# Kernel optimization log

Measured on AMD Instinct MI355X. Metric: run time of the kernel, lower is better.

## Reference

```python
import jax, jax.numpy as jnp
import numpy as np

N_QUBITS = 4
N_LAYERS = 2
ENT = [(i, (i + 1) % N_QUBITS) for i in range(N_QUBITS)]  # fixed entangling ring


def _ry(t):
    c, s = jnp.cos(t / 2), jnp.sin(t / 2)
    return jnp.stack([jnp.stack([c, -s]), jnp.stack([s, c])]).astype(jnp.complex64)


def _rx(t):
    c, s = jnp.cos(t / 2), jnp.sin(t / 2)
    return jnp.stack([jnp.stack([c + 0j, -1j * s]), jnp.stack([-1j * s, c + 0j])]).astype(jnp.complex64)


def _rz(t):
    e = jnp.exp(-0.5j * t.astype(jnp.complex64))
    z = jnp.zeros_like(e)
    return jnp.stack([jnp.stack([e, z]), jnp.stack([z, jnp.conj(e)])])


def _apply_1q(state, U, w):
    # state: (2,)*N_QUBITS; apply 2x2 U on wire w
    s = jnp.moveaxis(state, w, 0)
    s = jnp.tensordot(U, s, ((1,), (0,)))
    return jnp.moveaxis(s, 0, w)


def _cnot(state, c, t):
    s = jnp.moveaxis(state, (c, t), (0, 1))
    s = jnp.concatenate([s[:1], jnp.flip(s[1:], axis=1)], axis=0)
    return jnp.moveaxis(s, (0, 1), (c, t))


def _ansatz(state, vec, params):
    for i in range(N_QUBITS):
        state = _apply_1q(state, _ry(vec[i]), i)
    for l in range(N_LAYERS):
        for i in range(N_QUBITS):
            state = _apply_1q(state, _rx(params[l, i, 0]), i)
            state = _apply_1q(state, _ry(params[l, i, 1]), i)
            state = _apply_1q(state, _rz(params[l, i, 2]), i)
        for a_, b_ in ENT:
            state = _cnot(state, a_, b_)
    return state


def _adjoint_ansatz(state, vec, params):
    # inverse gates in reverse order
    for l in reversed(range(N_LAYERS)):
        for a_, b_ in reversed(ENT):
            state = _cnot(state, a_, b_)  # CNOT is self-inverse
        for i in reversed(range(N_QUBITS)):
            state = _apply_1q(state, _rz(-params[l, i, 2]), i)
            state = _apply_1q(state, _ry(-params[l, i, 1]), i)
            state = _apply_1q(state, _rx(-params[l, i, 0]), i)
    for i in reversed(range(N_QUBITS)):
        state = _apply_1q(state, _ry(-vec[i]), i)
    return state


def setup_inputs() -> dict:
    key = jax.random.key(0)
    k1, k2, k3 = jax.random.split(key, 3)
    a = jax.random.normal(k1, (1024, N_QUBITS), dtype=jnp.float32)
    b = jax.random.normal(k2, (1024, N_QUBITS), dtype=jnp.float32)
    params = jax.random.normal(k3, (N_LAYERS, N_QUBITS, 3), dtype=jnp.float32)
    return {"a": a, "b": b, "params": params}


def reference(a, b, params):
    def pair(x, y):
        psi = jnp.zeros((2,) * N_QUBITS, jnp.complex64).at[(0,) * N_QUBITS].set(1.0)
        psi = _ansatz(psi, x, params)
        psi = _adjoint_ansatz(psi, y, params)
        probs = jnp.abs(psi) ** 2
        # expval of PauliZ on wire 0: +1 for |0>, -1 for |1> on axis 0
        z = jnp.sum(probs[0]) - jnp.sum(probs[1])
        return jnp.abs(z)

    # Gram matrix [len(a), len(b)]
    return jax.vmap(lambda x: jax.vmap(lambda y: pair(x, y))(b))(a)
```

## Files before the change

kernel.cpp:

```cpp
#include <hip/hip_runtime.h>


#define NA 1024
#define NB 1024
#define KD 256
#define RT2 1.41421356237f

typedef __attribute__((ext_vector_type(8))) short bf16x8;
typedef __attribute__((ext_vector_type(4))) float f32x4;

__device__ __forceinline__ unsigned short f2bf(float x) {
    union { float f; unsigned u; } v; v.f = x;
    unsigned r = v.u + 0x7fffu + ((v.u >> 16) & 1u);
    return (unsigned short)(r >> 16);
}

__device__ __forceinline__ uint4 pack8(const float* f) {
    uint4 u;
    u.x = (unsigned)f2bf(f[0]) | ((unsigned)f2bf(f[1]) << 16);
    u.y = (unsigned)f2bf(f[2]) | ((unsigned)f2bf(f[3]) << 16);
    u.z = (unsigned)f2bf(f[4]) | ((unsigned)f2bf(f[5]) << 16);
    u.w = (unsigned)f2bf(f[6]) | ((unsigned)f2bf(f[7]) << 16);
    return u;
}

__device__ __forceinline__ void ry_gate(float* sr, float* si, int w, float t) {
    float s, c; __sincosf(0.5f * t, &s, &c);
    int st = 8 >> w;
    #pragma unroll
    for (int b = 0; b < 16; ++b) {
        if (b & st) continue;
        int j = b | st;
        float r0 = sr[b], i0 = si[b], r1 = sr[j], i1 = si[j];
        sr[b] = c * r0 - s * r1;  si[b] = c * i0 - s * i1;
        sr[j] = s * r0 + c * r1;  si[j] = s * i0 + c * i1;
    }
}

__device__ __forceinline__ void rx_gate(float* sr, float* si, int w, float t) {
    float s, c; __sincosf(0.5f * t, &s, &c);
    int st = 8 >> w;
    #pragma unroll
    for (int b = 0; b < 16; ++b) {
        if (b & st) continue;
        int j = b | st;
        float r0 = sr[b], i0 = si[b], r1 = sr[j], i1 = si[j];
        sr[b] = c * r0 + s * i1;  si[b] = c * i0 - s * r1;
        sr[j] = c * r1 + s * i0;  si[j] = c * i1 - s * r0;
    }
}

__device__ __forceinline__ void rz_gate(float* sr, float* si, int w, float t) {
    float s, c; __sincosf(0.5f * t, &s, &c);
    int st = 8 >> w;
    #pragma unroll
    for (int b = 0; b < 16; ++b) {
        if (b & st) continue;
        int j = b | st;
        float r0 = sr[b], i0 = si[b], r1 = sr[j], i1 = si[j];
        sr[b] = c * r0 + s * i0;  si[b] = c * i0 - s * r0;
        sr[j] = c * r1 - s * i1;  si[j] = c * i1 + s * r1;
    }
}

__device__ __forceinline__ void cnot_gate(float* sr, float* si, int cw, int tw) {
    int cs = 8 >> cw, ts = 8 >> tw;
    #pragma unroll
    for (int b = 0; b < 16; ++b) {
        if ((b & cs) && !(b & ts)) {
            int j = b | ts;
            float tr = sr[b]; sr[b] = sr[j]; sr[j] = tr;
            float ti = si[b]; si[b] = si[j]; si[j] = ti;
        }
    }
}

__device__ __forceinline__ void ansatz(float* sr, float* si, const float* vec, const float* P) {
    #pragma unroll
    for (int q = 0; q < 4; ++q) ry_gate(sr, si, q, vec[q]);
    #pragma unroll
    for (int l = 0; l < 2; ++l) {
        #pragma unroll
        for (int q = 0; q < 4; ++q) {
            rx_gate(sr, si, q, P[l * 12 + q * 3 + 0]);
            ry_gate(sr, si, q, P[l * 12 + q * 3 + 1]);
            rz_gate(sr, si, q, P[l * 12 + q * 3 + 2]);
        }
        cnot_gate(sr, si, 0, 1);
        cnot_gate(sr, si, 1, 2);
        cnot_gate(sr, si, 2, 3);
        cnot_gate(sr, si, 3, 0);
    }
}

__global__ __launch_bounds__(64) void qkm_phase1(
    const float* __restrict__ a, const float* __restrict__ b,
    const float* __restrict__ params,
    uint4* __restrict__ Qv, uint4* __restrict__ Mv) {
    float P[24];
    #pragma unroll
    for (int j = 0; j < 24; ++j) P[j] = params[j];
    int tid = threadIdx.x;
    int blk = blockIdx.x;

    if (blk < 128) {
        __shared__ float Wr[16][64];
        __shared__ float Wi[16][64];
        int g = tid >> 3, t = tid & 7;
        int y = (blk << 3) + g;
        float sr[16], si[16];
        #pragma unroll
        for (int k = 0; k < 16; ++k) { sr[k] = (k == 8 + t) ? 1.f : 0.f; si[k] = 0.f; }
        float vec[4];
        #pragma unroll
        for (int q = 0; q < 4; ++q) vec[q] = b[y * 4 + q];
        ansatz(sr, si, vec, P);
        #pragma unroll
        for (int l = 0; l < 16; ++l) { Wr[l][tid] = sr[l]; Wi[l][tid] = si[l]; }
        __syncthreads();
        int base = g << 3;
        #pragma unroll
        for (int kr = 0; kr < 2; ++kr) {
            int k = 2 * t + kr;
            float re[16], im[16];
            #pragma unroll
            for (int l = 0; l < 16; ++l) { re[l] = 0.f; im[l] = 0.f; }
            #pragma unroll
            for (int p2 = 0; p2 < 8; ++p2) {
                float wrk = Wr[k][base + p2], wik = Wi[k][base + p2];
                #pragma unroll
                for (int l = 0; l < 16; ++l) {
                    float wrl = Wr[l][base + p2], wil = Wi[l][base + p2];
                    re[l] += wrk * wrl + wik * wil;
                    im[l] += wil * wrk - wrl * wik;
                }
            }
            float row[16];
            #pragma unroll
            for (int l = 0; l < 16; ++l) {
                float off = (l < k) ? im[l] : re[l];
                row[l] = (l == k) ? (1.f - 2.f * re[l]) : (-2.f * RT2 * off);
            }
            uint4* d = Mv + y * 32 + k * 2;
            d[0] = pack8(row); d[1] = pack8(row + 8);
        }
    } else if (blk < 144) {
        int i = ((blk - 128) << 6) + tid;
        float sr[16], si[16];
        #pragma unroll
        for (int k = 0; k < 16; ++k) { sr[k] = (k == 0) ? 1.f : 0.f; si[k] = 0.f; }
        float vec[4];
        #pragma unroll
        for (int q = 0; q < 4; ++q) vec[q] = a[i * 4 + q];
        ansatz(sr, si, vec, P);
        #pragma unroll
        for (int k = 0; k < 16; ++k) {
            float rk = sr[k], ik = si[k];
            float row[16];
            #pragma unroll
            for (int l = 0; l < 16; ++l) {
                if (l < k)       row[l] = RT2 * (si[l] * rk - sr[l] * ik);
                else if (l == k) row[l] = rk * rk + ik * ik;
                else             row[l] = RT2 * (rk * sr[l] + ik * si[l]);
            }
            uint4* d = Qv + i * 32 + k * 2;
            d[0] = pack8(row); d[1] = pack8(row + 8);
        }
    }
}

__global__ __launch_bounds__(256) void qkm_phase2(
    const unsigned short* __restrict__ Q, const unsigned short* __restrict__ M,
    float* __restrict__ out) {
    int wave = threadIdx.x >> 6;
    int lane = threadIdx.x & 63;
    int blk = blockIdx.x;
    int xcd = blk & 7;
    int slot = blk >> 3;
    int bi = xcd * 2 + (slot >> 4);
    int bj = slot & 15;
    int wi = wave >> 1, wj = wave & 1;
    int row0 = bi * 64 + wi * 32;
    int col0 = bj * 64 + wj * 32;
    int m16 = lane & 15;
    int quad = lane >> 4;

    const unsigned short* q0 = Q + (size_t)(row0 + m16) * KD + quad * 8;
    const unsigned short* q1 = q0 + 16 * KD;
    const unsigned short* m0 = M + (size_t)(col0 + m16) * KD + quad * 8;
    const unsigned short* m1 = m0 + 16 * KD;

    f32x4 a00 = {0.f,0.f,0.f,0.f}, a01 = {0.f,0.f,0.f,0.f};
    f32x4 a10 = {0.f,0.f,0.f,0.f}, a11 = {0.f,0.f,0.f,0.f};
    #pragma unroll
    for (int kk = 0; kk < 8; ++kk) {
        bf16x8 qa = *(const bf16x8*)(q0 + kk * 32);
        bf16x8 qb = *(const bf16x8*)(q1 + kk * 32);
        bf16x8 ma = *(const bf16x8*)(m0 + kk * 32);
        bf16x8 mb = *(const bf16x8*)(m1 + kk * 32);
        a00 = __builtin_amdgcn_mfma_f32_16x16x32_bf16(qa, ma, a00, 0, 0, 0);
        a01 = __builtin_amdgcn_mfma_f32_16x16x32_bf16(qa, mb, a01, 0, 0, 0);
        a10 = __builtin_amdgcn_mfma_f32_16x16x32_bf16(qb, ma, a10, 0, 0, 0);
        a11 = __builtin_amdgcn_mfma_f32_16x16x32_bf16(qb, mb, a11, 0, 0, 0);
    }
    #pragma unroll
    for (int r = 0; r < 4; ++r) {
        int r0o = row0 + quad * 4 + r;
        int r1o = r0o + 16;
        out[r0o * NB + col0 + m16]      = fabsf(a00[r]);
        out[r0o * NB + col0 + 16 + m16] = fabsf(a01[r]);
        out[r1o * NB + col0 + m16]      = fabsf(a10[r]);
        out[r1o * NB + col0 + 16 + m16] = fabsf(a11[r]);
    }
}

extern "C" void kernel_launch(void* const* d_in, const int* in_sizes, int n_in,
                              void* d_out, int out_size, void* d_ws, size_t ws_size,
                              hipStream_t stream) {
    const float* a = (const float*)d_in[0];
    const float* b = (const float*)d_in[1];
    const float* params = (const float*)d_in[2];
    float* out = (float*)d_out;

    unsigned short* Q = (unsigned short*)d_ws;
    unsigned short* M = Q + (size_t)NA * KD;

    qkm_phase1<<<144, 64, 0, stream>>>(a, b, params, (uint4*)Q, (uint4*)M);
    qkm_phase2<<<256, 256, 0, stream>>>(Q, M, out);
}
```

Baseline: 70.83 us.

## Fuse state prep and MFMA gram into one kernel with LDS-resident Q/M tiles

Merges the two launches into a single kernel. Each 64x64 output tile block recomputes its own 64 a-rows and 64 b-column encodings and stores the bf16 Q/M operands in padded LDS instead of a global workspace. It also precomputes sincos of the parameters once per thread and reuses them across gates. This removes a kernel launch boundary and the global round trip of Q/M, at the cost of 16x redundant ansatz and M construction across blocks and a large dynamic LDS footprint that limits occupancy.

```diff
diff --git a/kernel.cpp b/kernel.cpp
--- a/kernel.cpp
+++ b/kernel.cpp
@@ -3,8 +3,10 @@
 
 #define NA 1024
 #define NB 1024
-#define KD 256
 #define RT2 1.41421356237f
+#define SW 577
+#define SQS 264
+#define LDS_BYTES (16*SW*4*2 + 64*SQS*2*2)
 
 typedef __attribute__((ext_vector_type(8))) short bf16x8;
 typedef __attribute__((ext_vector_type(4))) float f32x4;
@@ -24,8 +26,7 @@
     return u;
 }
 
-__device__ __forceinline__ void ry_gate(float* sr, float* si, int w, float t) {
-    float s, c; __sincosf(0.5f * t, &s, &c);
+__device__ __forceinline__ void ry_cs(float* sr, float* si, int w, float c, float s) {
     int st = 8 >> w;
     #pragma unroll
     for (int b = 0; b < 16; ++b) {
@@ -37,8 +38,7 @@
     }
 }
 
-__device__ __forceinline__ void rx_gate(float* sr, float* si, int w, float t) {
-    float s, c; __sincosf(0.5f * t, &s, &c);
+__device__ __forceinline__ void rx_cs(float* sr, float* si, int w, float c, float s) {
     int st = 8 >> w;
     #pragma unroll
     for (int b = 0; b < 16; ++b) {
@@ -50,8 +50,7 @@
     }
 }
 
-__device__ __forceinline__ void rz_gate(float* sr, float* si, int w, float t) {
-    float s, c; __sincosf(0.5f * t, &s, &c);
+__device__ __forceinline__ void rz_cs(float* sr, float* si, int w, float c, float s) {
     int st = 8 >> w;
     #pragma unroll
     for (int b = 0; b < 16; ++b) {
@@ -75,16 +74,18 @@
     }
 }
 
-__device__ __forceinline__ void ansatz(float* sr, float* si, const float* vec, const float* P) {
-    #pragma unroll
-    for (int q = 0; q < 4; ++q) ry_gate(sr, si, q, vec[q]);
+__device__ __forceinline__ void ansatz_cs(float* sr, float* si,
+                                          const float* vc, const float* vs,
+                                          const float* pc, const float* ps) {
+    #pragma unroll
+    for (int q = 0; q < 4; ++q) ry_cs(sr, si, q, vc[q], vs[q]);
     #pragma unroll
     for (int l = 0; l < 2; ++l) {
         #pragma unroll
         for (int q = 0; q < 4; ++q) {
-            rx_gate(sr, si, q, P[l * 12 + q * 3 + 0]);
-            ry_gate(sr, si, q, P[l * 12 + q * 3 + 1]);
-            rz_gate(sr, si, q, P[l * 12 + q * 3 + 2]);
+            rx_cs(sr, si, q, pc[l*12+q*3+0], ps[l*12+q*3+0]);
+            ry_cs(sr, si, q, pc[l*12+q*3+1], ps[l*12+q*3+1]);
+            rz_cs(sr, si, q, pc[l*12+q*3+2], ps[l*12+q*3+2]);
         }
         cnot_gate(sr, si, 0, 1);
         cnot_gate(sr, si, 1, 2);
@@ -93,66 +94,54 @@
     }
 }
 
-__global__ __launch_bounds__(64) void qkm_phase1(
+__global__ __launch_bounds__(256) void qkm_fused(
     const float* __restrict__ a, const float* __restrict__ b,
-    const float* __restrict__ params,
-    uint4* __restrict__ Qv, uint4* __restrict__ Mv) {
-    float P[24];
-    #pragma unroll
-    for (int j = 0; j < 24; ++j) P[j] = params[j];
+    const float* __restrict__ params, float* __restrict__ out) {
+    extern __shared__ char lds[];
+    float* Wr = (float*)lds;
+    float* Wi = Wr + 16 * SW;
+    unsigned short* SQ = (unsigned short*)(Wi + 16 * SW);
+    unsigned short* SM = SQ + 64 * SQS;
+
     int tid = threadIdx.x;
     int blk = blockIdx.x;
-
-    if (blk < 128) {
-        __shared__ float Wr[16][64];
-        __shared__ float Wi[16][64];
-        int g = tid >> 3, t = tid & 7;
-        int y = (blk << 3) + g;
+    int row_base = (blk >> 4) << 6;
+    int col_base = (blk & 15) << 6;
+
+    float pc[24], ps[24];
+    #pragma unroll
+    for (int j = 0; j < 24; ++j) __sincosf(0.5f * params[j], &ps[j], &pc[j]);
+
+    #pragma unroll
+    for (int rep = 0; rep < 2; ++rep) {
+        int s = tid + rep * 256;
+        int y = s >> 3, p = s & 7;
+        float4 bv = ((const float4*)b)[col_base + y];
+        float vc[4], vs[4];
+        __sincosf(0.5f * bv.x, &vs[0], &vc[0]);
+        __sincosf(0.5f * bv.y, &vs[1], &vc[1]);
+        __sincosf(0.5f * bv.z, &vs[2], &vc[2]);
+        __sincosf(0.5f * bv.w, &vs[3], &vc[3]);
         float sr[16], si[16];
         #pragma unroll
-        for (int k = 0; k < 16; ++k) { sr[k] = (k == 8 + t) ? 1.f : 0.f; si[k] = 0.f; }
-        float vec[4];
-        #pragma unroll
-        for (int q = 0; q < 4; ++q) vec[q] = b[y * 4 + q];
-        ansatz(sr, si, vec, P);
-        #pragma unroll
-        for (int l = 0; l < 16; ++l) { Wr[l][tid] = sr[l]; Wi[l][tid] = si[l]; }
-        __syncthreads();
-        int base = g << 3;
-        #pragma unroll
-        for (int kr = 0; kr < 2; ++kr) {
-            int k = 2 * t + kr;
-            float re[16], im[16];
-            #pragma unroll
-            for (int l = 0; l < 16; ++l) { re[l] = 0.f; im[l] = 0.f; }
-            #pragma unroll
-            for (int p2 = 0; p2 < 8; ++p2) {
-                float wrk = Wr[k][base + p2], wik = Wi[k][base + p2];
-                #pragma unroll
-                for (int l = 0; l < 16; ++l) {
-                    float wrl = Wr[l][base + p2], wil = Wi[l][base + p2];
-                    re[l] += wrk * wrl + wik * wil;
-                    im[l] += wil * wrk - wrl * wik;
-                }
-            }
-            float row[16];
-            #pragma unroll
-            for (int l = 0; l < 16; ++l) {
-                float off = (l < k) ? im[l] : re[l];
-                row[l] = (l == k) ? (1.f - 2.f * re[l]) : (-2.f * RT2 * off);
-            }
-            uint4* d = Mv + y * 32 + k * 2;
-            d[0] = pack8(row); d[1] = pack8(row + 8);
-        }
-    } else if (blk < 144) {
-        int i = ((blk - 128) << 6) + tid;
+        for (int k = 0; k < 16; ++k) { sr[k] = (k == 8 + p) ? 1.f : 0.f; si[k] = 0.f; }
+        ansatz_cs(sr, si, vc, vs, pc, ps);
+        int off = y * 9 + p;
+        #pragma unroll
+        for (int l = 0; l < 16; ++l) { Wr[l * SW + off] = sr[l]; Wi[l * SW + off] = si[l]; }
+    }
+
+    if (tid < 64) {
+        float4 av = ((const float4*)a)[row_base + tid];
+        float vc[4], vs[4];
+        __sincosf(0.5f * av.x, &vs[0], &vc[0]);
+        __sincosf(0.5f * av.y, &vs[1], &vc[1]);
+        __sincosf(0.5f * av.z, &vs[2], &vc[2]);
+        __sincosf(0.5f * av.w, &vs[3], &vc[3]);
         float sr[16], si[16];
         #pragma unroll
         for (int k = 0; k < 16; ++k) { sr[k] = (k == 0) ? 1.f : 0.f; si[k] = 0.f; }
-        float vec[4];
-        #pragma unroll
-        for (int q = 0; q < 4; ++q) vec[q] = a[i * 4 + q];
-        ansatz(sr, si, vec, P);
+        ansatz_cs(sr, si, vc, vs, pc, ps);
         #pragma unroll
         for (int k = 0; k < 16; ++k) {
             float rk = sr[k], ik = si[k];
@@ -163,32 +152,61 @@
                 else if (l == k) row[l] = rk * rk + ik * ik;
                 else             row[l] = RT2 * (rk * sr[l] + ik * si[l]);
             }
-            uint4* d = Qv + i * 32 + k * 2;
-            d[0] = pack8(row); d[1] = pack8(row + 8);
-        }
-    }
-}
-
-__global__ __launch_bounds__(256) void qkm_phase2(
-    const unsigned short* __restrict__ Q, const unsigned short* __restrict__ M,
-    float* __restrict__ out) {
-    int wave = threadIdx.x >> 6;
-    int lane = threadIdx.x & 63;
-    int blk = blockIdx.x;
-    int xcd = blk & 7;
-    int slot = blk >> 3;
-    int bi = xcd * 2 + (slot >> 4);
-    int bj = slot & 15;
+            *(uint4*)(SQ + tid * SQS + k * 16)     = pack8(row);
+            *(uint4*)(SQ + tid * SQS + k * 16 + 8) = pack8(row + 8);
+        }
+    }
+    __syncthreads();
+
+    {
+        int y = tid >> 2, t = tid & 3;
+        int base = y * 9;
+        #pragma unroll
+        for (int h = 0; h < 2; ++h) {
+            int k0 = 4 * t + 2 * h;
+            float re0[16], im0[16], re1[16], im1[16];
+            #pragma unroll
+            for (int l = 0; l < 16; ++l) { re0[l]=0.f; im0[l]=0.f; re1[l]=0.f; im1[l]=0.f; }
+            #pragma unroll
+            for (int p2 = 0; p2 < 8; ++p2) {
+                float wr0 = Wr[k0 * SW + base + p2],       wi0 = Wi[k0 * SW + base + p2];
+                float wr1 = Wr[(k0 + 1) * SW + base + p2], wi1 = Wi[(k0 + 1) * SW + base + p2];
+                #pragma unroll
+                for (int l = 0; l < 16; ++l) {
+                    float wrl = Wr[l * SW + base + p2], wil = Wi[l * SW + base + p2];
+                    re0[l] += wr0 * wrl + wi0 * wil;
+                    im0[l] += wil * wr0 - wrl * wi0;
+                    re1[l] += wr1 * wrl + wi1 * wil;
+                    im1[l] += wil * wr1 - wrl * wi1;
+                }
+            }
+            float row[16];
+            #pragma unroll
+            for (int l = 0; l < 16; ++l) {
+                float off = (l < k0) ? im0[l] : re0[l];
+                row[l] = (l == k0) ? (1.f - 2.f * re0[l]) : (-2.f * RT2 * off);
+            }
+            *(uint4*)(SM + y * SQS + k0 * 16)     = pack8(row);
+            *(uint4*)(SM + y * SQS + k0 * 16 + 8) = pack8(row + 8);
+            int k1 = k0 + 1;
+            #pragma unroll
+            for (int l = 0; l < 16; ++l) {
+                float off = (l < k1) ? im1[l] : re1[l];
+                row[l] = (l == k1) ? (1.f - 2.f * re1[l]) : (-2.f * RT2 * off);
+            }
+            *(uint4*)(SM + y * SQS + k1 * 16)     = pack8(row);
+            *(uint4*)(SM + y * SQS + k1 * 16 + 8) = pack8(row + 8);
+        }
+    }
+    __syncthreads();
+
+    int wave = tid >> 6, lane = tid & 63;
     int wi = wave >> 1, wj = wave & 1;
-    int row0 = bi * 64 + wi * 32;
-    int col0 = bj * 64 + wj * 32;
-    int m16 = lane & 15;
-    int quad = lane >> 4;
-
-    const unsigned short* q0 = Q + (size_t)(row0 + m16) * KD + quad * 8;
-    const unsigned short* q1 = q0 + 16 * KD;
-    const unsigned short* m0 = M + (size_t)(col0 + m16) * KD + quad * 8;
-    const unsigned short* m1 = m0 + 16 * KD;
+    int m16 = lane & 15, quad = lane >> 4;
+    const unsigned short* q0 = SQ + (wi * 32 + m16) * SQS + quad * 8;
+    const unsigned short* q1 = q0 + 16 * SQS;
+    const unsigned short* m0 = SM + (wj * 32 + m16) * SQS + quad * 8;
+    const unsigned short* m1 = m0 + 16 * SQS;
 
     f32x4 a00 = {0.f,0.f,0.f,0.f}, a01 = {0.f,0.f,0.f,0.f};
     f32x4 a10 = {0.f,0.f,0.f,0.f}, a11 = {0.f,0.f,0.f,0.f};
@@ -203,14 +221,15 @@
         a10 = __builtin_amdgcn_mfma_f32_16x16x32_bf16(qb, ma, a10, 0, 0, 0);
         a11 = __builtin_amdgcn_mfma_f32_16x16x32_bf16(qb, mb, a11, 0, 0, 0);
     }
+    int col = col_base + wj * 32 + m16;
     #pragma unroll
     for (int r = 0; r < 4; ++r) {
-        int r0o = row0 + quad * 4 + r;
+        int r0o = row_base + wi * 32 + quad * 4 + r;
         int r1o = r0o + 16;
-        out[r0o * NB + col0 + m16]      = fabsf(a00[r]);
-        out[r0o * NB + col0 + 16 + m16] = fabsf(a01[r]);
-        out[r1o * NB + col0 + m16]      = fabsf(a10[r]);
-        out[r1o * NB + col0 + 16 + m16] = fabsf(a11[r]);
+        out[r0o * NB + col]      = fabsf(a00[r]);
+        out[r0o * NB + col + 16] = fabsf(a01[r]);
+        out[r1o * NB + col]      = fabsf(a10[r]);
+        out[r1o * NB + col + 16] = fabsf(a11[r]);
     }
 }
 
@@ -222,9 +241,7 @@
     const float* params = (const float*)d_in[2];
     float* out = (float*)d_out;
 
-    unsigned short* Q = (unsigned short*)d_ws;
-    unsigned short* M = Q + (size_t)NA * KD;
-
-    qkm_phase1<<<144, 64, 0, stream>>>(a, b, params, (uint4*)Q, (uint4*)M);
-    qkm_phase2<<<256, 256, 0, stream>>>(Q, M, out);
-}
+    (void)hipFuncSetAttribute((const void*)qkm_fused,
+                              hipFuncAttributeMaxDynamicSharedMemorySize, LDS_BYTES);
+    qkm_fused<<<256, 256, LDS_BYTES, stream>>>(a, b, params, out);
+}
```

After: 78.73 us. +11.2%, slower.
